# Optimization experiments

Measured on AMD Instinct MI355X. Metric: run time of the kernel, lower is better.

## Reference

```python
import jax, jax.numpy as jnp
import numpy as np

B, S, V, E = 64, 100, 20000, 128
U, I = 10000, 20000


def setup_inputs() -> dict:
    key = jax.random.key(0)
    ks = jax.random.split(key, 12)
    initrange = 0.1
    return {
        "attr_item": jax.random.randint(ks[0], (B, S), 0, V, dtype=jnp.int32),
        "attr_tf_item": jax.random.uniform(ks[1], (B, S), dtype=jnp.float32),
        "attr_lens_item": jax.random.randint(ks[2], (B,), 1, S + 1, dtype=jnp.int32),
        "item_ids": jax.random.randint(ks[3], (B,), 0, I, dtype=jnp.int32),
        "attr_user": jax.random.randint(ks[4], (B, S), 0, V, dtype=jnp.int32),
        "attr_tf_user": jax.random.uniform(ks[5], (B, S), dtype=jnp.float32),
        "attr_lens_user": jax.random.randint(ks[6], (B,), 1, S + 1, dtype=jnp.int32),
        "user_ids": jax.random.randint(ks[7], (B,), 0, U, dtype=jnp.int32),
        "W_item": jax.random.uniform(ks[8], (V, E), jnp.float32, -initrange, initrange),
        "W_user": jax.random.uniform(ks[9], (V, E), jnp.float32, -initrange, initrange),
        "user_emb": jax.random.uniform(ks[10], (U, E), jnp.float32, -initrange, initrange),
        "item_emb": jax.random.uniform(ks[11], (I, E), jnp.float32, -initrange, initrange),
    }


def _cluster_logits(attr_ids, attr_tf, attr_lens, W):
    # attr_ids: [B,S] int, attr_tf: [B,S] float, attr_lens: [B] int, W: [V,E]
    seq = attr_ids.shape[1]
    mask = (jnp.arange(seq)[None, :] < attr_lens[:, None]).astype(attr_tf.dtype)  # [B,S]
    emb = W[attr_ids]                                   # [B,S,E]
    scores = jnp.einsum("bse,ve->bsv", emb, W)          # [B,S,V]
    cw = jax.nn.softmax(scores, axis=1)                 # softmax over seq dim (dim=1 in torch)
    # Algebraically identical to the [B,S,V,E] broadcast-mul-sum in the original:
    # logits[b,v] = sum_s (tf*mask)[b,s] * cw[b,s,v] * scores[b,s,v]
    return jnp.einsum("bs,bsv,bsv->bv", attr_tf * mask, cw, scores)


def reference(attr_item, attr_tf_item, attr_lens_item, item_ids,
              attr_user, attr_tf_user, attr_lens_user, user_ids,
              W_item, W_user, user_emb, item_emb):
    logits = _cluster_logits(attr_item, attr_tf_item, attr_lens_item, W_item)
    logits = logits + _cluster_logits(attr_user, attr_tf_user, attr_lens_user, W_user)
    logits = logits + user_emb[user_ids] @ W_user.T     # [B,V]
    logits = logits + item_emb[item_ids] @ W_item.T     # [B,V]
    return logits
```

## Files before the change

kernel.cpp:

```cpp
#include <hip/hip_runtime.h>

#define VDIM 20000
#define EDIM 128
#define BATCH 64
#define SEQ 100
#define BN 64
#define NVT 313
#define AROWS 112
#define ATILE (AROWS * EDIM)
#define GRID (NVT * 16)
#define GPX (GRID / 8)

typedef float f32x4 __attribute__((ext_vector_type(4)));
typedef short bf16x8 __attribute__((ext_vector_type(8)));
typedef unsigned short ushortx8 __attribute__((ext_vector_type(8)));

typedef __attribute__((address_space(1))) const unsigned int gas_u32;
typedef __attribute__((address_space(3))) unsigned int las_u32;

__device__ __forceinline__ void async16(unsigned short* lds, const unsigned short* g) {
  __builtin_amdgcn_global_load_lds((gas_u32*)g, (las_u32*)lds, 16, 0, 0);
}

__device__ __forceinline__ unsigned short f2bf(float f) {
  unsigned u = __builtin_bit_cast(unsigned, f);
  u += 0x7FFFu + ((u >> 16) & 1u);
  return (unsigned short)(u >> 16);
}

__global__ void prep_kernel(const float* __restrict__ Wi, const float* __restrict__ Wu,
                            const int* __restrict__ attr_item, const int* __restrict__ attr_user,
                            const int* __restrict__ item_ids, const int* __restrict__ user_ids,
                            const float* __restrict__ item_emb, const float* __restrict__ user_emb,
                            unsigned short* __restrict__ wbf, unsigned short* __restrict__ abf) {
  const int bid = blockIdx.x, t = threadIdx.x;
  if (bid < 2500) {
    const int c = bid & 1;
    const float* src = c ? Wu : Wi;
    unsigned short* dst = wbf + (size_t)c * (VDIM * EDIM);
    const int i0 = ((bid >> 1) * 256 + t) * 8;
    float4 a = *(const float4*)(src + i0);
    float4 b = *(const float4*)(src + i0 + 4);
    ushortx8 o;
    o[0] = f2bf(a.x); o[1] = f2bf(a.y); o[2] = f2bf(a.z); o[3] = f2bf(a.w);
    o[4] = f2bf(b.x); o[5] = f2bf(b.y); o[6] = f2bf(b.z); o[7] = f2bf(b.w);
    *(ushortx8*)(dst + i0) = o;
  } else {
    const int g = bid - 2500;
    const int b = g & 63, c = g >> 6;
    const int r = t >> 1, h = t & 1;
    if (r >= AROWS) return;
    const int* ids = c ? attr_user : attr_item;
    const float* W = c ? Wu : Wi;
    const float* demb = c ? user_emb : item_emb;
    const int* dids = c ? user_ids : item_ids;
    unsigned short* dst = abf + (size_t)(c * BATCH + b) * ATILE;
    const float* src = nullptr;
    if (r < SEQ)       src = W + (size_t)ids[b * SEQ + r] * EDIM;
    else if (r == SEQ) src = demb + (size_t)dids[b] * EDIM;
    if (src) {
      #pragma unroll
      for (int k = 0; k < 8; ++k) {
        const int jj = h * 8 + k;
        const int j = jj ^ (r & 15);
        float4 a  = *(const float4*)(src + j * 8);
        float4 bb = *(const float4*)(src + j * 8 + 4);
        ushortx8 o;
        o[0] = f2bf(a.x);  o[1] = f2bf(a.y);  o[2] = f2bf(a.z);  o[3] = f2bf(a.w);
        o[4] = f2bf(bb.x); o[5] = f2bf(bb.y); o[6] = f2bf(bb.z); o[7] = f2bf(bb.w);
        *(ushortx8*)(dst + (r * 16 + jj) * 8) = o;
      }
    } else {
      ushortx8 z = {0, 0, 0, 0, 0, 0, 0, 0};
      #pragma unroll
      for (int k = 0; k < 8; ++k) *(ushortx8*)(dst + (r * 16 + h * 8 + k) * 8) = z;
    }
  }
}

__global__ __launch_bounds__(256, 4)
void main_kernel(const unsigned short* __restrict__ wbf, const unsigned short* __restrict__ abf,
                 const float* __restrict__ tf_item, const int* __restrict__ lens_item,
                 const float* __restrict__ tf_user, const int* __restrict__ lens_user,
                 float* __restrict__ out) {
  __shared__ __align__(16) unsigned short sA[ATILE];
  __shared__ float sDen[2][2][BN];
  __shared__ float sNum[2][2][BN];
  __shared__ float sDir[2][BN];
  __shared__ float sTF[2][4][128];
  __shared__ int   sLen[2][4];
  __shared__ float sRes[4][BN];

  const int t = threadIdx.x;
  const int bid = blockIdx.x;
  const int p = (bid & 7) * GPX + (bid >> 3);
  const int v0 = (p >> 4) * BN;
  const int bg4 = (p & 15) * 4;
  const int lane = t & 63, wave = t >> 6;
  const int wm = wave >> 1, wn = wave & 1;
  const int quad = lane >> 4, l15 = lane & 15;

  #pragma unroll
  for (int k = t; k < 1024; k += 256) {
    const int c = k >> 9, bi = (k >> 7) & 3, si = k & 127;
    float w = 0.f;
    if (si < SEQ) w = (c ? tf_user : tf_item)[(bg4 + bi) * SEQ + si];
    sTF[c][bi][si] = w;
  }
  if (t < 8) sLen[t >> 2][t & 3] = ((t >= 4) ? lens_user : lens_item)[bg4 + (t & 3)];

  bf16x8 breg[2][4];
  #pragma unroll
  for (int nt = 0; nt < 2; ++nt) {
    const int v = v0 + wn * 32 + nt * 16 + l15;
    const unsigned short* pb = wbf + (size_t)v * EDIM + quad * 8;
    const bool ok = (v < VDIM);
    #pragma unroll
    for (int ks = 0; ks < 4; ++ks) {
      bf16x8 z = {0, 0, 0, 0, 0, 0, 0, 0};
      breg[nt][ks] = ok ? *(const bf16x8*)(pb + ks * 32) : z;
    }
  }

  {
    const unsigned short* gb = abf + (size_t)bg4 * ATILE;
    #pragma unroll
    for (int i = 0; i < 7; ++i)
      async16(&sA[(i * 256 + wave * 64) * 8], gb + (size_t)(i * 256 + t) * 8);
  }

  #pragma unroll 1
  for (int s = 0; s < 8; ++s) {
    const int c = s >> 2, it = s & 3, buf = s & 1;

    __syncthreads();

    if (s > 0 && t < BN) {
      const int ps = s - 1, pp = ps & 1, pit = ps & 3;
      float den = sDen[pp][0][t] + sDen[pp][1][t];
      float num = sNum[pp][0][t] + sNum[pp][1][t];
      const float dir = sDir[pp][t];
      den -= 11.f + __expf(dir);
      const float val = num * __builtin_amdgcn_rcpf(den) + dir;
      if (ps < 4) sRes[pit][t] = val;
      else {
        const int v = v0 + t;
        if (v < VDIM) out[(size_t)(bg4 + pit) * VDIM + v] = sRes[pit][t] + val;
      }
    }

    f32x4 acc[4][2];
    #pragma unroll
    for (int mt = 0; mt < 4; ++mt)
      #pragma unroll
      for (int nt = 0; nt < 2; ++nt) { f32x4 z = {0.f, 0.f, 0.f, 0.f}; acc[mt][nt] = z; }

    const unsigned char* pA = (const unsigned char*)&sA[0];
    #pragma unroll
    for (int ks = 0; ks < 4; ++ks) {
      const int j = ks * 4 + quad;
      const int sw = ((j ^ l15) << 4);
      bf16x8 af[3];
      #pragma unroll
      for (int mt = 0; mt < 3; ++mt)
        af[mt] = *(const bf16x8*)(pA + (wm * 64 + mt * 16 + l15) * 256 + sw);
      #pragma unroll
      for (int mt = 0; mt < 3; ++mt)
        #pragma unroll
        for (int nt = 0; nt < 2; ++nt)
          acc[mt][nt] = __builtin_amdgcn_mfma_f32_16x16x32_bf16(af[mt], breg[nt][ks], acc[mt][nt], 0, 0, 0);
      if (wm == 0) {
        const bf16x8 a3 = *(const bf16x8*)(pA + (3 * 16 + l15) * 256 + sw);
        #pragma unroll
        for (int nt = 0; nt < 2; ++nt)
          acc[3][nt] = __builtin_amdgcn_mfma_f32_16x16x32_bf16(a3, breg[nt][ks], acc[3][nt], 0, 0, 0);
      }
    }

    __syncthreads();

    if (s < 7) {
      const int ns = s + 1;
      const unsigned short* gb = abf + (size_t)((ns >> 2) * BATCH + bg4 + (ns & 3)) * ATILE;
      #pragma unroll
      for (int i = 0; i < 7; ++i)
        async16(&sA[(i * 256 + wave * 64) * 8], gb + (size_t)(i * 256 + t) * 8);
    }
    if (s == 3) {
      const unsigned short* wb1 = wbf + (size_t)VDIM * EDIM;
      #pragma unroll
      for (int nt = 0; nt < 2; ++nt) {
        const int v = v0 + wn * 32 + nt * 16 + l15;
        const unsigned short* pb = wb1 + (size_t)v * EDIM + quad * 8;
        const bool ok = (v < VDIM);
        #pragma unroll
        for (int ks = 0; ks < 4; ++ks) {
          bf16x8 z = {0, 0, 0, 0, 0, 0, 0, 0};
          breg[nt][ks] = ok ? *(const bf16x8*)(pb + ks * 32) : z;
        }
      }
    }

    const int lenb = sLen[c][it];
    float wv[4][4];
    #pragma unroll
    for (int mt = 0; mt < 4; ++mt)
      #pragma unroll
      for (int r = 0; r < 4; ++r) {
        const int row = wm * 64 + mt * 16 + quad * 4 + r;
        wv[mt][r] = (row < lenb) ? sTF[c][it][row & 127] : 0.f;
      }

    #pragma unroll
    for (int nt = 0; nt < 2; ++nt) {
      float den = 0.f, num = 0.f;
      #pragma unroll
      for (int mt = 0; mt < 3; ++mt)
        #pragma unroll
        for (int r = 0; r < 4; ++r) {
          const float v = acc[mt][nt][r];
          const float e = __expf(v);
          den += e;
          num = fmaf(wv[mt][r], e * v, num);
        }
      if (wm == 0) {
        #pragma unroll
        for (int r = 0; r < 4; ++r) {
          const float v = acc[3][nt][r];
          const float e = __expf(v);
          den += e;
          num = fmaf(wv[3][r], e * v, num);
        }
      }
      den += __shfl_xor(den, 16, 64);
      den += __shfl_xor(den, 32, 64);
      num += __shfl_xor(num, 16, 64);
      num += __shfl_xor(num, 32, 64);
      const int col = wn * 32 + nt * 16 + l15;
      if (quad == 0) {
        sDen[buf][wm][col] = den;
        sNum[buf][wm][col] = num;
      }
      if (wm == 1 && quad == 1) sDir[buf][col] = acc[2][nt][0];
    }
  }

  __syncthreads();

  if (t < BN) {
    float den = sDen[1][0][t] + sDen[1][1][t];
    float num = sNum[1][0][t] + sNum[1][1][t];
    const float dir = sDir[1][t];
    den -= 11.f + __expf(dir);
    const float val = num * __builtin_amdgcn_rcpf(den) + dir;
    const int v = v0 + t;
    if (v < VDIM) out[(size_t)(bg4 + 3) * VDIM + v] = sRes[3][t] + val;
  }
}

extern "C" void kernel_launch(void* const* d_in, const int* in_sizes, int n_in,
                              void* d_out, int out_size, void* d_ws, size_t ws_size,
                              hipStream_t stream) {
  const int*   attr_item = (const int*)d_in[0];
  const float* tf_item   = (const float*)d_in[1];
  const int*   lens_item = (const int*)d_in[2];
  const int*   item_ids  = (const int*)d_in[3];
  const int*   attr_user = (const int*)d_in[4];
  const float* tf_user   = (const float*)d_in[5];
  const int*   lens_user = (const int*)d_in[6];
  const int*   user_ids  = (const int*)d_in[7];
  const float* W_item    = (const float*)d_in[8];
  const float* W_user    = (const float*)d_in[9];
  const float* user_emb  = (const float*)d_in[10];
  const float* item_emb  = (const float*)d_in[11];
  float* out = (float*)d_out;

  unsigned short* wbf = (unsigned short*)d_ws;
  unsigned short* abf = wbf + (size_t)2 * VDIM * EDIM;

  prep_kernel<<<dim3(2500 + 128), 256, 0, stream>>>(W_item, W_user, attr_item, attr_user,
                                                    item_ids, user_ids, item_emb, user_emb,
                                                    wbf, abf);
  main_kernel<<<dim3(GRID), 256, 0, stream>>>(wbf, abf, tf_item, lens_item,
                                              tf_user, lens_user, out);
}
```

Measured before the change: 243.4 us.

## Widen vocab tile to 96 columns and pack the softmax epilogue math

Each block now covers 96 vocabulary columns instead of 64, so each wave holds three B fragments. Every A tile staged in LDS therefore feeds more MFMAs, and fewer blocks reload the same A tiles. The exp/sum epilogue now uses packed v_pk_mul/add/fma and raw v_exp_f32 with a log2(e) prescale. The length mask is folded into the staged tf weights, so sLen and the per-row compare go away. The cost is higher register pressure: launch bounds drop to 3 blocks per SIMD and there are fewer total blocks, which may reduce occupancy and latency hiding.

Measured after the change: 229.0 us. 5.9% less time.

```diff
diff --git a/kernel.cpp b/kernel.cpp
--- a/kernel.cpp
+++ b/kernel.cpp
@@ -4,14 +4,15 @@
 #define EDIM 128
 #define BATCH 64
 #define SEQ 100
-#define BN 64
-#define NVT 313
+#define BN 96
+#define NVT 209
 #define AROWS 112
 #define ATILE (AROWS * EDIM)
 #define GRID (NVT * 16)
 #define GPX (GRID / 8)
 
 typedef float f32x4 __attribute__((ext_vector_type(4)));
+typedef float f32x2 __attribute__((ext_vector_type(2)));
 typedef short bf16x8 __attribute__((ext_vector_type(8)));
 typedef unsigned short ushortx8 __attribute__((ext_vector_type(8)));
 
@@ -27,6 +28,20 @@
   u += 0x7FFFu + ((u >> 16) & 1u);
   return (unsigned short)(u >> 16);
 }
+
+__device__ __forceinline__ f32x2 pk_mul(f32x2 a, f32x2 b) {
+  f32x2 d; asm("v_pk_mul_f32 %0, %1, %2" : "=v"(d) : "v"(a), "v"(b)); return d;
+}
+__device__ __forceinline__ f32x2 pk_add(f32x2 a, f32x2 b) {
+  f32x2 d; asm("v_pk_add_f32 %0, %1, %2" : "=v"(d) : "v"(a), "v"(b)); return d;
+}
+__device__ __forceinline__ f32x2 pk_fma(f32x2 a, f32x2 b, f32x2 c) {
+  f32x2 d; asm("v_pk_fma_f32 %0, %1, %2, %3" : "=v"(d) : "v"(a), "v"(b), "v"(c)); return d;
+}
+__device__ __forceinline__ float fexp2(float x) {
+  float d; asm("v_exp_f32 %0, %1" : "=v"(d) : "v"(x)); return d;
+}
+#define L2E_BITS 0x3FB8AA3Bu
 
 __global__ void prep_kernel(const float* __restrict__ Wi, const float* __restrict__ Wu,
                             const int* __restrict__ attr_item, const int* __restrict__ attr_user,
@@ -78,7 +93,7 @@
   }
 }
 
-__global__ __launch_bounds__(256, 4)
+__global__ __launch_bounds__(256, 3)
 void main_kernel(const unsigned short* __restrict__ wbf, const unsigned short* __restrict__ abf,
                  const float* __restrict__ tf_item, const int* __restrict__ lens_item,
                  const float* __restrict__ tf_user, const int* __restrict__ lens_user,
@@ -87,8 +102,7 @@
   __shared__ float sDen[2][2][BN];
   __shared__ float sNum[2][2][BN];
   __shared__ float sDir[2][BN];
-  __shared__ float sTF[2][4][128];
-  __shared__ int   sLen[2][4];
+  __shared__ __align__(16) float sTF[2][4][128];
   __shared__ float sRes[4][BN];
 
   const int t = threadIdx.x;
@@ -99,20 +113,22 @@
   const int lane = t & 63, wave = t >> 6;
   const int wm = wave >> 1, wn = wave & 1;
   const int quad = lane >> 4, l15 = lane & 15;
+  const float L2E = __builtin_bit_cast(float, L2E_BITS);
+  const f32x2 L2E2 = {L2E, L2E};
 
   #pragma unroll
   for (int k = t; k < 1024; k += 256) {
     const int c = k >> 9, bi = (k >> 7) & 3, si = k & 127;
+    const int lb = (c ? lens_user : lens_item)[bg4 + bi];
     float w = 0.f;
-    if (si < SEQ) w = (c ? tf_user : tf_item)[(bg4 + bi) * SEQ + si];
+    if (si < lb) w = (c ? tf_user : tf_item)[(bg4 + bi) * SEQ + si];
     sTF[c][bi][si] = w;
   }
-  if (t < 8) sLen[t >> 2][t & 3] = ((t >= 4) ? lens_user : lens_item)[bg4 + (t & 3)];
-
-  bf16x8 breg[2][4];
+
+  bf16x8 breg[3][4];
   #pragma unroll
-  for (int nt = 0; nt < 2; ++nt) {
-    const int v = v0 + wn * 32 + nt * 16 + l15;
+  for (int nt = 0; nt < 3; ++nt) {
+    const int v = v0 + wn * 48 + nt * 16 + l15;
     const unsigned short* pb = wbf + (size_t)v * EDIM + quad * 8;
     const bool ok = (v < VDIM);
     #pragma unroll
@@ -131,7 +147,7 @@
 
   #pragma unroll 1
   for (int s = 0; s < 8; ++s) {
-    const int c = s >> 2, it = s & 3, buf = s & 1;
+    const int cc = s >> 2, it = s & 3, buf = s & 1;
 
     __syncthreads();
 
@@ -140,7 +156,8 @@
       float den = sDen[pp][0][t] + sDen[pp][1][t];
       float num = sNum[pp][0][t] + sNum[pp][1][t];
       const float dir = sDir[pp][t];
-      den -= 11.f + __expf(dir);
+      const float dirE = fexp2(dir * L2E);
+      den -= 11.f + dirE;
       const float val = num * __builtin_amdgcn_rcpf(den) + dir;
       if (ps < 4) sRes[pit][t] = val;
       else {
@@ -149,11 +166,11 @@
       }
     }
 
-    f32x4 acc[4][2];
+    f32x4 acc[4][3];
     #pragma unroll
     for (int mt = 0; mt < 4; ++mt)
       #pragma unroll
-      for (int nt = 0; nt < 2; ++nt) { f32x4 z = {0.f, 0.f, 0.f, 0.f}; acc[mt][nt] = z; }
+      for (int nt = 0; nt < 3; ++nt) { f32x4 z = {0.f, 0.f, 0.f, 0.f}; acc[mt][nt] = z; }
 
     const unsigned char* pA = (const unsigned char*)&sA[0];
     #pragma unroll
@@ -167,12 +184,12 @@
       #pragma unroll
       for (int mt = 0; mt < 3; ++mt)
         #pragma unroll
-        for (int nt = 0; nt < 2; ++nt)
+        for (int nt = 0; nt < 3; ++nt)
           acc[mt][nt] = __builtin_amdgcn_mfma_f32_16x16x32_bf16(af[mt], breg[nt][ks], acc[mt][nt], 0, 0, 0);
       if (wm == 0) {
         const bf16x8 a3 = *(const bf16x8*)(pA + (3 * 16 + l15) * 256 + sw);
         #pragma unroll
-        for (int nt = 0; nt < 2; ++nt)
+        for (int nt = 0; nt < 3; ++nt)
           acc[3][nt] = __builtin_amdgcn_mfma_f32_16x16x32_bf16(a3, breg[nt][ks], acc[3][nt], 0, 0, 0);
       }
     }
@@ -189,8 +206,8 @@
     if (s == 3) {
       const unsigned short* wb1 = wbf + (size_t)VDIM * EDIM;
       #pragma unroll
-      for (int nt = 0; nt < 2; ++nt) {
-        const int v = v0 + wn * 32 + nt * 16 + l15;
+      for (int nt = 0; nt < 3; ++nt) {
+        const int v = v0 + wn * 48 + nt * 16 + l15;
         const unsigned short* pb = wb1 + (size_t)v * EDIM + quad * 8;
         const bool ok = (v < VDIM);
         #pragma unroll
@@ -201,42 +218,47 @@
       }
     }
 
-    const int lenb = sLen[c][it];
-    float wv[4][4];
-    #pragma unroll
-    for (int mt = 0; mt < 4; ++mt)
-      #pragma unroll
-      for (int r = 0; r < 4; ++r) {
-        const int row = wm * 64 + mt * 16 + quad * 4 + r;
-        wv[mt][r] = (row < lenb) ? sTF[c][it][row & 127] : 0.f;
-      }
-
-    #pragma unroll
-    for (int nt = 0; nt < 2; ++nt) {
-      float den = 0.f, num = 0.f;
-      #pragma unroll
-      for (int mt = 0; mt < 3; ++mt)
-        #pragma unroll
-        for (int r = 0; r < 4; ++r) {
-          const float v = acc[mt][nt][r];
-          const float e = __expf(v);
-          den += e;
-          num = fmaf(wv[mt][r], e * v, num);
-        }
-      if (wm == 0) {
-        #pragma unroll
-        for (int r = 0; r < 4; ++r) {
-          const float v = acc[3][nt][r];
-          const float e = __expf(v);
-          den += e;
-          num = fmaf(wv[3][r], e * v, num);
-        }
-      }
+    f32x2 wlo[4], whi[4];
+    #pragma unroll
+    for (int mt = 0; mt < 4; ++mt) {
+      const int row0 = wm * 64 + mt * 16 + quad * 4;
+      const f32x4 w4 = *(const f32x4*)&sTF[cc][it][row0];
+      f32x2 a = {w4[0], w4[1]}; f32x2 b = {w4[2], w4[3]};
+      wlo[mt] = a; whi[mt] = b;
+    }
+
+    #pragma unroll
+    for (int nt = 0; nt < 3; ++nt) {
+      f32x2 den2 = {0.f, 0.f}, num2 = {0.f, 0.f};
+
+      #define EPAIRS(MT)                                                  \
+      {                                                                   \
+        const f32x4 a4 = acc[MT][nt];                                     \
+        const f32x2 vlo = {a4[0], a4[1]};                                 \
+        const f32x2 vhi = {a4[2], a4[3]};                                 \
+        const f32x2 mlo = pk_mul(vlo, L2E2);                              \
+        const f32x2 mhi = pk_mul(vhi, L2E2);                              \
+        f32x2 elo, ehi;                                                   \
+        elo[0] = fexp2(mlo[0]); elo[1] = fexp2(mlo[1]);                   \
+        ehi[0] = fexp2(mhi[0]); ehi[1] = fexp2(mhi[1]);                   \
+        den2 = pk_add(den2, elo);                                         \
+        den2 = pk_add(den2, ehi);                                         \
+        num2 = pk_fma(wlo[MT], pk_mul(elo, vlo), num2);                   \
+        num2 = pk_fma(whi[MT], pk_mul(ehi, vhi), num2);                   \
+      }
+      EPAIRS(0)
+      EPAIRS(1)
+      EPAIRS(2)
+      if (wm == 0) EPAIRS(3)
+      #undef EPAIRS
+
+      float den = den2[0] + den2[1];
+      float num = num2[0] + num2[1];
       den += __shfl_xor(den, 16, 64);
       den += __shfl_xor(den, 32, 64);
       num += __shfl_xor(num, 16, 64);
       num += __shfl_xor(num, 32, 64);
-      const int col = wn * 32 + nt * 16 + l15;
+      const int col = wn * 48 + nt * 16 + l15;
       if (quad == 0) {
         sDen[buf][wm][col] = den;
         sNum[buf][wm][col] = num;
@@ -251,7 +273,8 @@
     float den = sDen[1][0][t] + sDen[1][1][t];
     float num = sNum[1][0][t] + sNum[1][1][t];
     const float dir = sDir[1][t];
-    den -= 11.f + __expf(dir);
+    const float dirE = fexp2(dir * L2E);
+    den -= 11.f + dirE;
     const float val = num * __builtin_amdgcn_rcpf(den) + dir;
     const int v = v0 + t;
     if (v < VDIM) out[(size_t)(bg4 + 3) * VDIM + v] = sRes[3][t] + val;
```
